# Optimization experiments

Measured on AMD Instinct MI355X. Metric: run time of the kernel, lower is better.

Reference implementation:

```python
import jax, jax.numpy as jnp
import numpy as np

N = 100000
E = 1600000
D_IN = 128
D_H = 128
BN_EPS = 1e-5


def setup_inputs() -> dict:
    key = jax.random.key(0)
    ks = jax.random.split(key, 8)
    x = jax.random.normal(ks[0], (N, D_IN), dtype=jnp.float32)
    edge_index = jax.random.randint(ks[1], (2, E), 0, N, dtype=jnp.int64)
    # MLP params (Linear stores weight as [out, in])
    lim1 = 1.0 / np.sqrt(D_IN)
    W1 = jax.random.uniform(ks[2], (D_H, D_IN), minval=-lim1, maxval=lim1, dtype=jnp.float32)
    b1 = jax.random.uniform(ks[3], (D_H,), minval=-lim1, maxval=lim1, dtype=jnp.float32)
    gamma = jnp.ones((D_H,), dtype=jnp.float32)
    beta = jnp.zeros((D_H,), dtype=jnp.float32)
    lim2 = 1.0 / np.sqrt(D_H)
    W2 = jax.random.uniform(ks[4], (D_H, D_H), minval=-lim2, maxval=lim2, dtype=jnp.float32)
    b2 = jax.random.uniform(ks[5], (D_H,), minval=-lim2, maxval=lim2, dtype=jnp.float32)
    eps = jnp.float32(0.0)  # trainable eps parameter, init 0
    return {"x": x, "edge_index": edge_index, "eps": eps, "W1": W1, "b1": b1,
            "gamma": gamma, "beta": beta, "W2": W2, "b2": b2}


def reference(x, edge_index, eps, W1, b1, gamma, beta, W2, b2):
    src = edge_index[0]
    dst = edge_index[1]
    # Augmented edges = original + reversed + self-loops.
    # aggr[dst] += x[src]; aggr[src] += x[dst]; aggr[i] += x[i]
    aggr = jnp.zeros_like(x).at[dst].add(x[src]).at[src].add(x[dst]) + x
    h = (1.0 + eps) * x + aggr              # [N, D_IN]
    h = h @ W1.T + b1                        # [N, D_H]
    # BatchNorm1d in training mode: batch stats, biased variance
    mean = jnp.mean(h, axis=0)
    var = jnp.mean(jnp.square(h - mean), axis=0)
    h = gamma * (h - mean) * jax.lax.rsqrt(var + BN_EPS) + beta
    h = jax.nn.relu(h)
    return h @ W2.T + b2                     # [N, D_H]
```

## Files before the change

kernel.cpp:

```cpp
#include <hip/hip_runtime.h>
#include <hip/hip_fp16.h>

#define N_NODES 100000
#define EDGES   1600000
#define D       128
#define BN_EPS  1e-5f
#define TM      64
#define NT      ((N_NODES + TM - 1) / TM)
#define GGRID   782
#define NB      782
#define SLOT    4800
#define SBS     13
#define L1E     8
#define L1TILE  (256 * L1E)
#define GBLKS   1536
#define GWAVES  (GBLKS * 4)
#define NREP    32

typedef __attribute__((ext_vector_type(8))) short short8;
typedef __attribute__((ext_vector_type(4))) float f32x4;

__device__ __forceinline__ unsigned short bf_hi(float f) {
    unsigned u = __float_as_uint(f);
    unsigned t = u + 0x7FFF + ((u >> 16) & 1);
    return (unsigned short)(t >> 16);
}
__device__ __forceinline__ float bf_val(unsigned short h) {
    return __uint_as_float(((unsigned)h) << 16);
}
__device__ __forceinline__ void split8(const float* __restrict__ p, short8* hi, short8* lo) {
    short8 h, l;
#pragma unroll
    for (int i = 0; i < 8; ++i) {
        float f = p[i];
        unsigned short hh = bf_hi(f);
        ((unsigned short*)&h)[i] = (short)hh;
        ((unsigned short*)&l)[i] = (short)bf_hi(f - bf_val(hh));
    }
    *hi = h; *lo = l;
}

__launch_bounds__(256)
__global__ void fused_pg(const float* __restrict__ x,
                         const float* __restrict__ W1,
                         __half* __restrict__ yh,
                         const int* __restrict__ ei, int* __restrict__ gcur,
                         int* __restrict__ pairs) {
    __shared__ unsigned short sH[TM][136];
    __shared__ unsigned short sL[TM][136];
    const int tid = threadIdx.x;

    if (blockIdx.x >= GGRID) {
        int* cnt   = (int*)&sH[0][0];
        int* cbase = cnt + NB;
        for (int i = tid; i < NB; i += 256) cnt[i] = 0;
        __syncthreads();

        int bbA[L1E], rrA[L1E], pkA[L1E];
        int bbB[L1E], rrB[L1E], pkB[L1E];
        const int t0 = (blockIdx.x - GGRID) * L1TILE + tid;
#pragma unroll
        for (int j = 0; j < L1E; ++j) {
            int t = t0 + j * 256;
            bbA[j] = -1;
            bbB[j] = -1;
            if (t < EDGES) {
                int s = ei[t];
                int d = ei[EDGES + t];
                bbA[j] = d >> 7;
                pkA[j] = ((d & 127) << 17) | s;
                rrA[j] = atomicAdd(&cnt[bbA[j]], 1);
                bbB[j] = s >> 7;
                pkB[j] = ((s & 127) << 17) | d;
                rrB[j] = atomicAdd(&cnt[bbB[j]], 1);
            }
        }
        __syncthreads();
        for (int i = tid; i < NB; i += 256) {
            int c = cnt[i];
            cbase[i] = c ? (i * SLOT + atomicAdd(&gcur[i], c)) : 0;
        }
        __syncthreads();
#pragma unroll
        for (int j = 0; j < L1E; ++j) {
            if (bbA[j] >= 0) {
                pairs[cbase[bbA[j]] + rrA[j]] = pkA[j];
                pairs[cbase[bbB[j]] + rrB[j]] = pkB[j];
            }
        }
        return;
    }

    const int wv  = tid >> 6;
    const int ln  = tid & 63;
    const int lc  = ln & 15;
    const int qd  = ln >> 4;
    const int sr  = tid >> 5;
    const int sc4 = tid & 31;

    short8 Bh[4][2], Bl[4][2];
#pragma unroll
    for (int kk = 0; kk < 4; ++kk)
#pragma unroll
        for (int tl = 0; tl < 2; ++tl) {
            int woff = (wv * 32 + tl * 16 + lc) * D + kk * 32 + qd * 8;
            split8(W1 + woff, &Bh[kk][tl], &Bl[kk][tl]);
        }

    float4 pf[8];
    int tile = blockIdx.x;
#pragma unroll
    for (int i = 0; i < 8; ++i) {
        int gr = tile * TM + sr + i * 8;
        pf[i] = make_float4(0.f, 0.f, 0.f, 0.f);
        if (gr < N_NODES)
            pf[i] = *(const float4*)(x + (long long)gr * D + sc4 * 4);
    }

    while (tile < NT) {
#pragma unroll
        for (int i = 0; i < 8; ++i) {
            float4 v = pf[i];
            unsigned short h0 = bf_hi(v.x), h1b = bf_hi(v.y), h2 = bf_hi(v.z), h3 = bf_hi(v.w);
            unsigned short l0 = bf_hi(v.x - bf_val(h0)), l1 = bf_hi(v.y - bf_val(h1b));
            unsigned short l2 = bf_hi(v.z - bf_val(h2)), l3 = bf_hi(v.w - bf_val(h3));
            int r = sr + i * 8;
            *(uint2*)&sH[r][sc4 * 4] = make_uint2((unsigned)h0 | ((unsigned)h1b << 16),
                                                  (unsigned)h2 | ((unsigned)h3 << 16));
            *(uint2*)&sL[r][sc4 * 4] = make_uint2((unsigned)l0 | ((unsigned)l1 << 16),
                                                  (unsigned)l2 | ((unsigned)l3 << 16));
        }
        __syncthreads();
        int nxt = tile + GGRID;
        if (nxt < NT) {
#pragma unroll
            for (int i = 0; i < 8; ++i) {
                int gr = nxt * TM + sr + i * 8;
                pf[i] = make_float4(0.f, 0.f, 0.f, 0.f);
                if (gr < N_NODES)
                    pf[i] = *(const float4*)(x + (long long)gr * D + sc4 * 4);
            }
        }

        f32x4 acc[4][2];
#pragma unroll
        for (int m = 0; m < 4; ++m)
#pragma unroll
            for (int tl = 0; tl < 2; ++tl) acc[m][tl] = (f32x4){0.f, 0.f, 0.f, 0.f};

#pragma unroll
        for (int kk = 0; kk < 4; ++kk) {
#pragma unroll
            for (int m = 0; m < 4; ++m) {
                short8 ah = *(const short8*)&sH[m * 16 + lc][kk * 32 + qd * 8];
                short8 al = *(const short8*)&sL[m * 16 + lc][kk * 32 + qd * 8];
#pragma unroll
                for (int tl = 0; tl < 2; ++tl) {
                    acc[m][tl] = __builtin_amdgcn_mfma_f32_16x16x32_bf16(ah, Bh[kk][tl], acc[m][tl], 0, 0, 0);
                    acc[m][tl] = __builtin_amdgcn_mfma_f32_16x16x32_bf16(al, Bh[kk][tl], acc[m][tl], 0, 0, 0);
                    acc[m][tl] = __builtin_amdgcn_mfma_f32_16x16x32_bf16(ah, Bl[kk][tl], acc[m][tl], 0, 0, 0);
                }
            }
        }

        const int row0 = tile * TM;
#pragma unroll
        for (int m = 0; m < 4; ++m)
#pragma unroll
            for (int tl = 0; tl < 2; ++tl) {
                int col = wv * 32 + tl * 16 + lc;
#pragma unroll
                for (int r = 0; r < 4; ++r) {
                    int grow = row0 + m * 16 + qd * 4 + r;
                    if (grow < N_NODES)
                        yh[(long long)grow * D + col] = __float2half(acc[m][tl][r]);
                }
            }
        __syncthreads();
        tile = nxt;
    }
}

__launch_bounds__(256)
__global__ void bucket_fill(int* __restrict__ pairs, const int* __restrict__ gcur,
                            int* __restrict__ ofs, int* __restrict__ oen) {
    __shared__ int sP[SLOT];
    __shared__ int cnt2[128 * SBS];
    __shared__ int lc[128];
    const int b    = blockIdx.x;
    const int tid  = threadIdx.x;
    const int base = b * SLOT;
    const int m    = min(gcur[b], SLOT);
    for (int i = tid; i < m; i += 256) sP[i] = pairs[base + i];
    for (int i = tid; i < 128 * SBS; i += 256) cnt2[i] = 0;
    __syncthreads();
    for (int i = tid; i < m; i += 256) {
        int p = sP[i];
        atomicAdd(&cnt2[(p >> 17) * SBS + ((p & 0x1FFFF) >> 13)], 1);
    }
    __syncthreads();
    int v = 0;
    if (tid < 128) {
#pragma unroll
        for (int j = 0; j < SBS; ++j) v += cnt2[tid * SBS + j];
        lc[tid] = v;
    }
    __syncthreads();
    for (int d = 1; d < 128; d <<= 1) {
        int u = (tid >= d && tid < 128) ? lc[tid - d] : 0;
        __syncthreads();
        if (tid < 128) lc[tid] += u;
        __syncthreads();
    }
    if (tid < 128) {
        int run = base + lc[tid] - v;
        const int n = (b << 7) + tid;
        if (n < N_NODES) { ofs[n] = run; oen[n] = run + v; }
#pragma unroll
        for (int j = 0; j < SBS; ++j) {
            int c = cnt2[tid * SBS + j];
            cnt2[tid * SBS + j] = run;
            run += c;
        }
    }
    __syncthreads();
    for (int i = tid; i < m; i += 256) {
        int p = sP[i];
        int src = p & 0x1FFFF;
        int r = atomicAdd(&cnt2[(p >> 17) * SBS + (src >> 13)], 1);
        pairs[r] = src;
    }
}

__launch_bounds__(256)
__global__ void gather_aggr(const __half* __restrict__ yh,
                            const int* __restrict__ adj, const int* __restrict__ ofs,
                            const int* __restrict__ oen, const float* __restrict__ eps_p,
                            const float* __restrict__ b1,
                            float* __restrict__ h1, float* __restrict__ stats) {
    const int wv   = threadIdx.x >> 6;
    const int lane = threadIdx.x & 63;
    const int wave = blockIdx.x * 4 + wv;
    const __half2* xp = (const __half2*)yh;
    const float sc = 2.0f + eps_p[0];
    const float2 b1c = ((const float2*)b1)[lane];
    float sx = 0.f, sy = 0.f, qx = 0.f, qy = 0.f;

    for (int node = wave; node < N_NODES; node += GWAVES) {
        int b = ofs[node];
        int e = oen[node];
        float ax = 0.f, ay = 0.f;
        int i = b;
        for (; i + 8 <= e; i += 8) {
            int n0 = adj[i],     n1 = adj[i + 1], n2 = adj[i + 2], n3 = adj[i + 3];
            int n4 = adj[i + 4], n5 = adj[i + 5], n6 = adj[i + 6], n7 = adj[i + 7];
            __half2 v0 = xp[(unsigned)n0 * 64u + lane];
            __half2 v1 = xp[(unsigned)n1 * 64u + lane];
            __half2 v2 = xp[(unsigned)n2 * 64u + lane];
            __half2 v3 = xp[(unsigned)n3 * 64u + lane];
            __half2 v4 = xp[(unsigned)n4 * 64u + lane];
            __half2 v5 = xp[(unsigned)n5 * 64u + lane];
            __half2 v6 = xp[(unsigned)n6 * 64u + lane];
            __half2 v7 = xp[(unsigned)n7 * 64u + lane];
            float2 f0 = __half22float2(v0);
            float2 f1 = __half22float2(v1);
            float2 f2 = __half22float2(v2);
            float2 f3 = __half22float2(v3);
            float2 f4 = __half22float2(v4);
            float2 f5 = __half22float2(v5);
            float2 f6 = __half22float2(v6);
            float2 f7 = __half22float2(v7);
            ax += ((f0.x + f1.x) + (f2.x + f3.x)) + ((f4.x + f5.x) + (f6.x + f7.x));
            ay += ((f0.y + f1.y) + (f2.y + f3.y)) + ((f4.y + f5.y) + (f6.y + f7.y));
        }
        for (; i + 4 <= e; i += 4) {
            int n0 = adj[i], n1 = adj[i + 1], n2 = adj[i + 2], n3 = adj[i + 3];
            __half2 v0 = xp[(unsigned)n0 * 64u + lane];
            __half2 v1 = xp[(unsigned)n1 * 64u + lane];
            __half2 v2 = xp[(unsigned)n2 * 64u + lane];
            __half2 v3 = xp[(unsigned)n3 * 64u + lane];
            float2 f0 = __half22float2(v0);
            float2 f1 = __half22float2(v1);
            float2 f2 = __half22float2(v2);
            float2 f3 = __half22float2(v3);
            ax += (f0.x + f1.x) + (f2.x + f3.x);
            ay += (f0.y + f1.y) + (f2.y + f3.y);
        }
        for (; i < e; ++i) {
            __half2 v = xp[(unsigned)adj[i] * 64u + lane];
            float2 f = __half22float2(v);
            ax += f.x;
            ay += f.y;
        }
        float2 ys = __half22float2(xp[(unsigned)node * 64u + lane]);
        float ox = fmaf(sc, ys.x, ax) + b1c.x;
        float oy = fmaf(sc, ys.y, ay) + b1c.y;
        ((float2*)h1)[(long long)node * 64 + lane] = make_float2(ox, oy);
        sx += ox; sy += oy;
        qx += ox * ox; qy += oy * oy;
    }

    __shared__ float4 red[4][64];
    red[wv][lane] = make_float4(sx, sy, qx, qy);
    __syncthreads();
    if (wv == 0) {
        float4 a = red[0][lane], b4 = red[1][lane], c = red[2][lane], d4 = red[3][lane];
        float fx = (a.x + b4.x) + (c.x + d4.x);
        float fy = (a.y + b4.y) + (c.y + d4.y);
        float gx = (a.z + b4.z) + (c.z + d4.z);
        float gy = (a.w + b4.w) + (c.w + d4.w);
        float* st = stats + (blockIdx.x & (NREP - 1)) * 256;
        atomicAdd(&st[2 * lane],       fx);
        atomicAdd(&st[2 * lane + 1],   fy);
        atomicAdd(&st[128 + 2 * lane],     gx);
        atomicAdd(&st[128 + 2 * lane + 1], gy);
    }
}

__launch_bounds__(256)
__global__ void gemm2_mfma(float* __restrict__ h1out,
                           const float* __restrict__ W2,
                           const float* __restrict__ b2, const float* __restrict__ stats,
                           const float* __restrict__ gamma, const float* __restrict__ beta) {
    __shared__ unsigned short sH[TM][136];
    __shared__ unsigned short sL[TM][136];
    __shared__ float sScale[128];
    __shared__ float sShift[128];
    const int tid = threadIdx.x;
    const int wv  = tid >> 6;
    const int ln  = tid & 63;
    const int lc  = ln & 15;
    const int qd  = ln >> 4;
    const int sr  = tid >> 5;
    const int sc4 = tid & 31;

    if (tid < 128) {
        float s = 0.f, q = 0.f;
#pragma unroll
        for (int r = 0; r < NREP; ++r) {
            s += stats[r * 256 + tid];
            q += stats[r * 256 + 128 + tid];
        }
        float mean = s * (1.0f / N_NODES);
        float var  = fmaxf(q * (1.0f / N_NODES) - mean * mean, 0.0f);
        float sc   = gamma[tid] * rsqrtf(var + BN_EPS);
        sScale[tid] = sc;
        sShift[tid] = beta[tid] - mean * sc;
    }

    short8 Bh[4][2], Bl[4][2];
#pragma unroll
    for (int kk = 0; kk < 4; ++kk)
#pragma unroll
        for (int tl = 0; tl < 2; ++tl) {
            int woff = (wv * 32 + tl * 16 + lc) * D + kk * 32 + qd * 8;
            split8(W2 + woff, &Bh[kk][tl], &Bl[kk][tl]);
        }
    float bb[2];
    bb[0] = b2[wv * 32 + lc];
    bb[1] = b2[wv * 32 + 16 + lc];

    __syncthreads();

    float4 pf[8];
    int tile = blockIdx.x;
#pragma unroll
    for (int i = 0; i < 8; ++i) {
        int gr = tile * TM + sr + i * 8;
        pf[i] = make_float4(0.f, 0.f, 0.f, 0.f);
        if (gr < N_NODES)
            pf[i] = *(const float4*)(h1out + (long long)gr * D + sc4 * 4);
    }

    while (tile < NT) {
        float4 scv = *(const float4*)&sScale[sc4 * 4];
        float4 shv = *(const float4*)&sShift[sc4 * 4];
#pragma unroll
        for (int i = 0; i < 8; ++i) {
            int gr = tile * TM + sr + i * 8;
            float4 v = pf[i];
            if (gr < N_NODES) {
                v.x = fmaxf(0.f, fmaf(v.x, scv.x, shv.x));
                v.y = fmaxf(0.f, fmaf(v.y, scv.y, shv.y));
                v.z = fmaxf(0.f, fmaf(v.z, scv.z, shv.z));
                v.w = fmaxf(0.f, fmaf(v.w, scv.w, shv.w));
            } else {
                v = make_float4(0.f, 0.f, 0.f, 0.f);
            }
            unsigned short h0 = bf_hi(v.x), h1b = bf_hi(v.y), h2 = bf_hi(v.z), h3 = bf_hi(v.w);
            unsigned short l0 = bf_hi(v.x - bf_val(h0)), l1 = bf_hi(v.y - bf_val(h1b));
            unsigned short l2 = bf_hi(v.z - bf_val(h2)), l3 = bf_hi(v.w - bf_val(h3));
            int r = sr + i * 8;
            *(uint2*)&sH[r][sc4 * 4] = make_uint2((unsigned)h0 | ((unsigned)h1b << 16),
                                                  (unsigned)h2 | ((unsigned)h3 << 16));
            *(uint2*)&sL[r][sc4 * 4] = make_uint2((unsigned)l0 | ((unsigned)l1 << 16),
                                                  (unsigned)l2 | ((unsigned)l3 << 16));
        }
        __syncthreads();
        int nxt = tile + GGRID;
        if (nxt < NT) {
#pragma unroll
            for (int i = 0; i < 8; ++i) {
                int gr = nxt * TM + sr + i * 8;
                pf[i] = make_float4(0.f, 0.f, 0.f, 0.f);
                if (gr < N_NODES)
                    pf[i] = *(const float4*)(h1out + (long long)gr * D + sc4 * 4);
            }
        }

        f32x4 acc[4][2];
#pragma unroll
        for (int m = 0; m < 4; ++m)
#pragma unroll
            for (int tl = 0; tl < 2; ++tl) acc[m][tl] = (f32x4){0.f, 0.f, 0.f, 0.f};

#pragma unroll
        for (int kk = 0; kk < 4; ++kk) {
#pragma unroll
            for (int m = 0; m < 4; ++m) {
                short8 ah = *(const short8*)&sH[m * 16 + lc][kk * 32 + qd * 8];
                short8 al = *(const short8*)&sL[m * 16 + lc][kk * 32 + qd * 8];
#pragma unroll
                for (int tl = 0; tl < 2; ++tl) {
                    acc[m][tl] = __builtin_amdgcn_mfma_f32_16x16x32_bf16(ah, Bh[kk][tl], acc[m][tl], 0, 0, 0);
                    acc[m][tl] = __builtin_amdgcn_mfma_f32_16x16x32_bf16(al, Bh[kk][tl], acc[m][tl], 0, 0, 0);
                    acc[m][tl] = __builtin_amdgcn_mfma_f32_16x16x32_bf16(ah, Bl[kk][tl], acc[m][tl], 0, 0, 0);
                }
            }
        }

        const int row0 = tile * TM;
#pragma unroll
        for (int m = 0; m < 4; ++m)
#pragma unroll
            for (int tl = 0; tl < 2; ++tl) {
                int col = wv * 32 + tl * 16 + lc;
#pragma unroll
                for (int r = 0; r < 4; ++r) {
                    int grow = row0 + m * 16 + qd * 4 + r;
                    if (grow < N_NODES)
                        h1out[(long long)grow * D + col] = acc[m][tl][r] + bb[tl];
                }
            }
        __syncthreads();
        tile = nxt;
    }
}

extern "C" void kernel_launch(void* const* d_in, const int* in_sizes, int n_in,
                              void* d_out, int out_size, void* d_ws, size_t ws_size,
                              hipStream_t stream) {
    const float* x     = (const float*)d_in[0];
    const int*   ei    = (const int*)d_in[1];
    const float* eps_p = (const float*)d_in[2];
    const float* W1    = (const float*)d_in[3];
    const float* b1    = (const float*)d_in[4];
    const float* gamma = (const float*)d_in[5];
    const float* beta  = (const float*)d_in[6];
    const float* W2    = (const float*)d_in[7];
    const float* b2    = (const float*)d_in[8];

    __half* yh   = (__half*)d_ws;
    float*  stats = (float*)(yh + (long long)N_NODES * D);
    int*    gcur  = (int*)(stats + NREP * 256);
    int*    ofs   = gcur + 1024;
    int*    oen   = ofs + N_NODES;
    int*    pairs = (int*)(oen + N_NODES);
    int*    adj   = pairs;

    float* out = (float*)d_out;

    hipMemsetAsync(stats, 0, (NREP * 256 + 1024) * sizeof(int), stream);

    {
        fused_pg<<<GGRID + 782, 256, 0, stream>>>(x, W1, yh, ei, gcur, pairs);
    }
    {
        bucket_fill<<<NB, 256, 0, stream>>>(pairs, gcur, ofs, oen);
    }
    {
        gather_aggr<<<GBLKS, 256, 0, stream>>>(yh, adj, ofs, oen, eps_p, b1, out, stats);
    }
    {
        gemm2_mfma<<<GGRID, 256, 0, stream>>>(out, W2, b2, stats, gamma, beta);
    }
}
```

Measured before the change: 338.1 us.

## Simplify bucket fill, widen gather unroll to 16, raise gather grid

Bucket_fill drops the per-node sub-bucketing by source range and uses a single per-node counter, so the adjacency is no longer sorted by source within each node. The gather loop is unrolled to 16 outstanding neighbour loads instead of 8 to expose more memory-level parallelism. The gather grid also grows from 1536 to 2048 blocks. The sub-bucket removal cuts LDS work but may hurt cache locality in the gather, and the deeper unroll raises register pressure.

```diff
diff --git a/kernel.cpp b/kernel.cpp
--- a/kernel.cpp
+++ b/kernel.cpp
@@ -10,10 +10,9 @@
 #define GGRID   782
 #define NB      782
 #define SLOT    4800
-#define SBS     13
 #define L1E     8
 #define L1TILE  (256 * L1E)
-#define GBLKS   1536
+#define GBLKS   2048
 #define GWAVES  (GBLKS * 4)
 #define NREP    32
 
@@ -185,50 +184,35 @@
 __global__ void bucket_fill(int* __restrict__ pairs, const int* __restrict__ gcur,
                             int* __restrict__ ofs, int* __restrict__ oen) {
     __shared__ int sP[SLOT];
-    __shared__ int cnt2[128 * SBS];
     __shared__ int lc[128];
+    __shared__ int cur[128];
     const int b    = blockIdx.x;
     const int tid  = threadIdx.x;
     const int base = b * SLOT;
     const int m    = min(gcur[b], SLOT);
     for (int i = tid; i < m; i += 256) sP[i] = pairs[base + i];
-    for (int i = tid; i < 128 * SBS; i += 256) cnt2[i] = 0;
+    if (tid < 128) lc[tid] = 0;
+    __syncthreads();
+    for (int i = tid; i < m; i += 256) atomicAdd(&lc[sP[i] >> 17], 1);
+    __syncthreads();
+    int v = (tid < 128) ? lc[tid] : 0;
+    for (int d = 1; d < 128; d <<= 1) {
+        int u = (tid >= d && tid < 128) ? lc[tid - d] : 0;
+        __syncthreads();
+        if (tid < 128) lc[tid] += u;
+        __syncthreads();
+    }
+    if (tid < 128) {
+        int abs0 = base + lc[tid] - v;
+        cur[tid] = abs0;
+        const int n = (b << 7) + tid;
+        if (n < N_NODES) { ofs[n] = abs0; oen[n] = abs0 + v; }
+    }
     __syncthreads();
     for (int i = tid; i < m; i += 256) {
         int p = sP[i];
-        atomicAdd(&cnt2[(p >> 17) * SBS + ((p & 0x1FFFF) >> 13)], 1);
-    }
-    __syncthreads();
-    int v = 0;
-    if (tid < 128) {
-#pragma unroll
-        for (int j = 0; j < SBS; ++j) v += cnt2[tid * SBS + j];
-        lc[tid] = v;
-    }
-    __syncthreads();
-    for (int d = 1; d < 128; d <<= 1) {
-        int u = (tid >= d && tid < 128) ? lc[tid - d] : 0;
-        __syncthreads();
-        if (tid < 128) lc[tid] += u;
-        __syncthreads();
-    }
-    if (tid < 128) {
-        int run = base + lc[tid] - v;
-        const int n = (b << 7) + tid;
-        if (n < N_NODES) { ofs[n] = run; oen[n] = run + v; }
-#pragma unroll
-        for (int j = 0; j < SBS; ++j) {
-            int c = cnt2[tid * SBS + j];
-            cnt2[tid * SBS + j] = run;
-            run += c;
-        }
-    }
-    __syncthreads();
-    for (int i = tid; i < m; i += 256) {
-        int p = sP[i];
-        int src = p & 0x1FFFF;
-        int r = atomicAdd(&cnt2[(p >> 17) * SBS + (src >> 13)], 1);
-        pairs[r] = src;
+        int r = atomicAdd(&cur[p >> 17], 1);
+        pairs[r] = p & 0x1FFFF;
     }
 }
 
@@ -251,27 +235,19 @@
         int e = oen[node];
         float ax = 0.f, ay = 0.f;
         int i = b;
-        for (; i + 8 <= e; i += 8) {
-            int n0 = adj[i],     n1 = adj[i + 1], n2 = adj[i + 2], n3 = adj[i + 3];
-            int n4 = adj[i + 4], n5 = adj[i + 5], n6 = adj[i + 6], n7 = adj[i + 7];
-            __half2 v0 = xp[(unsigned)n0 * 64u + lane];
-            __half2 v1 = xp[(unsigned)n1 * 64u + lane];
-            __half2 v2 = xp[(unsigned)n2 * 64u + lane];
-            __half2 v3 = xp[(unsigned)n3 * 64u + lane];
-            __half2 v4 = xp[(unsigned)n4 * 64u + lane];
-            __half2 v5 = xp[(unsigned)n5 * 64u + lane];
-            __half2 v6 = xp[(unsigned)n6 * 64u + lane];
-            __half2 v7 = xp[(unsigned)n7 * 64u + lane];
-            float2 f0 = __half22float2(v0);
-            float2 f1 = __half22float2(v1);
-            float2 f2 = __half22float2(v2);
-            float2 f3 = __half22float2(v3);
-            float2 f4 = __half22float2(v4);
-            float2 f5 = __half22float2(v5);
-            float2 f6 = __half22float2(v6);
-            float2 f7 = __half22float2(v7);
-            ax += ((f0.x + f1.x) + (f2.x + f3.x)) + ((f4.x + f5.x) + (f6.x + f7.x));
-            ay += ((f0.y + f1.y) + (f2.y + f3.y)) + ((f4.y + f5.y) + (f6.y + f7.y));
+        for (; i + 16 <= e; i += 16) {
+            int n[16];
+#pragma unroll
+            for (int j = 0; j < 16; ++j) n[j] = adj[i + j];
+            __half2 v[16];
+#pragma unroll
+            for (int j = 0; j < 16; ++j) v[j] = xp[(unsigned)n[j] * 64u + lane];
+#pragma unroll
+            for (int j = 0; j < 16; ++j) {
+                float2 f = __half22float2(v[j]);
+                ax += f.x;
+                ay += f.y;
+            }
         }
         for (; i + 4 <= e; i += 4) {
             int n0 = adj[i], n1 = adj[i + 1], n2 = adj[i + 2], n3 = adj[i + 3];
```

Result: slower. 360.0 us (+6.5%).
